# Performance work log

Hardware: AMD Instinct MI355X
Metric: run time of the kernel (lower is better)

The kernel has to match this reference:

```python
import jax, jax.numpy as jnp
import numpy as np

D = 2048; HQ = 16; HKV = 4; HD = 128
E = 8; F = 2048; FS = 11008; TOPK = 2
B = 2; S = 1024
EPS = 1e-6
NEG = -1e9


def setup_inputs() -> dict:
    key = jax.random.key(0)
    ks = jax.random.split(key, 16)
    p = lambda k, shape: jax.random.normal(k, shape, jnp.float32) * 0.02
    # rotary tables (rotate-half convention): [S, HD]
    pos = jnp.arange(S, dtype=jnp.float32)[:, None]
    inv = 1.0 / (10000.0 ** (jnp.arange(0, HD, 2, dtype=jnp.float32) / HD))
    ang = pos * inv[None, :]
    cos = jnp.concatenate([jnp.cos(ang), jnp.cos(ang)], axis=-1)
    sin = jnp.concatenate([jnp.sin(ang), jnp.sin(ang)], axis=-1)
    return dict(
        x=jax.random.normal(ks[0], (B, S, D), jnp.float32),
        rope_cos=cos, rope_sin=sin,
        attn_norm_w=jnp.ones((D,), jnp.float32),
        ffn_norm_w=jnp.ones((D,), jnp.float32),
        wq=p(ks[1], (D, HQ * HD)), bq=jnp.zeros((HQ * HD,), jnp.float32),
        wk=p(ks[2], (D, HKV * HD)), bk=jnp.zeros((HKV * HD,), jnp.float32),
        wv=p(ks[3], (D, HKV * HD)), bv=jnp.zeros((HKV * HD,), jnp.float32),
        wo=p(ks[4], (HQ * HD, D)),
        router_w=p(ks[5], (D, E)),
        w_gate=p(ks[6], (E, D, F)), w_up=p(ks[7], (E, D, F)), w_down=p(ks[8], (E, F, D)),
        ws_gate=p(ks[9], (D, FS)), ws_up=p(ks[10], (D, FS)), ws_down=p(ks[11], (FS, D)),
    )


def rmsnorm(x, w):
    return x * jax.lax.rsqrt(jnp.mean(x * x, axis=-1, keepdims=True) + EPS) * w


def rotate_half(x):
    x1, x2 = jnp.split(x, 2, axis=-1)
    return jnp.concatenate([-x2, x1], axis=-1)


def reference(x, rope_cos, rope_sin, attn_norm_w, ffn_norm_w,
              wq, bq, wk, bk, wv, bv, wo, router_w,
              w_gate, w_up, w_down, ws_gate, ws_up, ws_down):
    b, s, d = x.shape
    # ---- attention sublayer ----
    h = rmsnorm(x, attn_norm_w)
    q = (h @ wq + bq).reshape(b, s, HQ, HD)
    k = (h @ wk + bk).reshape(b, s, HKV, HD)
    v = (h @ wv + bv).reshape(b, s, HKV, HD)
    cos = rope_cos[None, :, None, :]
    sin = rope_sin[None, :, None, :]
    q = q * cos + rotate_half(q) * sin
    k = k * cos + rotate_half(k) * sin
    rep = HQ // HKV
    k = jnp.repeat(k, rep, axis=2)   # [b,s,HQ,HD]
    v = jnp.repeat(v, rep, axis=2)
    scores = jnp.einsum('bqhd,bkhd->bhqk', q, k) / np.sqrt(HD).astype(np.float32)
    causal = jnp.tril(jnp.ones((s, s), bool))
    scores = jnp.where(causal[None, None], scores, NEG)
    attn = jax.nn.softmax(scores, axis=-1)
    o = jnp.einsum('bhqk,bkhd->bqhd', attn, v).reshape(b, s, HQ * HD) @ wo
    new_k, new_v = k, v
    x = x + o
    # ---- MoE sublayer ----
    hn = rmsnorm(x, ffn_norm_w).reshape(b * s, d)   # [T,D]
    logits = hn @ router_w                           # [T,E]
    probs = jax.nn.softmax(logits, axis=-1)
    topv, topi = jax.lax.top_k(probs, TOPK)          # [T,K]
    topv = topv / jnp.sum(topv, axis=-1, keepdims=True)
    onehot = jax.nn.one_hot(topi, E, dtype=hn.dtype)  # [T,K,E]
    wdense = jnp.einsum('tke,tk->te', onehot, topv)   # sparse combine weights [T,E]
    g = jnp.einsum('td,edf->tef', hn, w_gate)
    u = jnp.einsum('td,edf->tef', hn, w_up)
    y = jnp.einsum('tef,efd->ted', jax.nn.silu(g) * u, w_down)
    routed = jnp.einsum('ted,te->td', y, wdense)
    shared = (jax.nn.silu(hn @ ws_gate) * (hn @ ws_up)) @ ws_down
    moe = (routed + shared).reshape(b, s, d)
    # load-balancing aux loss (Switch/Mixtral convention)
    frac = jnp.mean(onehot, axis=(0, 1))             # fraction dispatched per expert
    pmean = jnp.mean(probs, axis=0)
    aux_loss = E * jnp.sum(frac * pmean)
    out = x + moe
    return out, (new_k, new_v), aux_loss
```

## Files before the change

kernel.cpp:

```cpp
#include <hip/hip_runtime.h>

typedef unsigned short u16;
typedef unsigned int u32;
typedef unsigned long long u64;
typedef __attribute__((ext_vector_type(4))) unsigned short u16x4;
typedef __attribute__((ext_vector_type(8))) unsigned short u16x8;
typedef __attribute__((ext_vector_type(4))) float f32x4;
typedef __attribute__((ext_vector_type(8))) __bf16 bf16x8;

#define DD 2048
#define TT 2048
#define FSH 11008

__device__ __forceinline__ float bf2f(u16 u) {
  union { u32 i; float f; } v; v.i = ((u32)u) << 16; return v.f;
}
__device__ __forceinline__ u16 f2bf(float f) {
  union { float f; u32 i; } v; v.f = f;
  u32 r = v.i + 0x7fffu + ((v.i >> 16) & 1u);
  return (u16)(r >> 16);
}
__device__ __forceinline__ void gld16(const void* g, void* l) {
  __builtin_amdgcn_global_load_lds((const __attribute__((address_space(1))) void*)g,
                                   (__attribute__((address_space(3))) void*)l, 16, 0, 0);
}

#define MFMA16(d, a, b) d = __builtin_amdgcn_mfma_f32_16x16x32_bf16(a, b, d, 0, 0, 0)

__device__ __forceinline__ void ttile(const float* __restrict__ Wm, u16* __restrict__ Wtm,
                                      int R, int C, int n0, int k0, u16* tile, int t) {
#pragma unroll
  for (int p = 0; p < 4; ++p) {
    const int kk = (t >> 4) + p * 16;
    const int nn = (t & 15) * 4;
    float4 v = *(const float4*)(Wm + (size_t)(k0 + kk) * C + n0 + nn);
    const float vv[4] = {v.x, v.y, v.z, v.w};
#pragma unroll
    for (int j = 0; j < 4; ++j) {
      const int n = nn + j;
      tile[n * 80 + (kk ^ (((n >> 2) & 7) << 3))] = f2bf(vv[j]);
    }
  }
  __syncthreads();
#pragma unroll
  for (int p = 0; p < 2; ++p) {
    const int n = (t >> 3) + p * 32;
    const int c = t & 7;
    u16x8 v = *(const u16x8*)(tile + n * 80 + ((c * 8) ^ (((n >> 2) & 7) << 3)));
    *(u16x8*)(Wtm + (size_t)(n0 + n) * R + k0 + c * 8) = v;
  }
}

__global__ __launch_bounds__(256) void rmsnorm_k(const float* __restrict__ x,
                                                 const float* __restrict__ w,
                                                 u16* __restrict__ out) {
  const int t = threadIdx.x;
  const float* xr = x + (size_t)blockIdx.x * DD;
  float4 a = *(const float4*)(xr + t * 8);
  float4 b = *(const float4*)(xr + t * 8 + 4);
  float ss = a.x*a.x + a.y*a.y + a.z*a.z + a.w*a.w
           + b.x*b.x + b.y*b.y + b.z*b.z + b.w*b.w;
#pragma unroll
  for (int m = 1; m < 64; m <<= 1) ss += __shfl_xor(ss, m);
  __shared__ float red[4];
  if ((t & 63) == 0) red[t >> 6] = ss;
  __syncthreads();
  float sc = rsqrtf((red[0] + red[1] + red[2] + red[3]) * (1.f / DD) + 1e-6f);
  float4 wa = *(const float4*)(w + t * 8);
  float4 wb = *(const float4*)(w + t * 8 + 4);
  u16x8 o;
  o[0] = f2bf(a.x * sc * wa.x); o[1] = f2bf(a.y * sc * wa.y);
  o[2] = f2bf(a.z * sc * wa.z); o[3] = f2bf(a.w * sc * wa.w);
  o[4] = f2bf(b.x * sc * wb.x); o[5] = f2bf(b.y * sc * wb.y);
  o[6] = f2bf(b.z * sc * wb.z); o[7] = f2bf(b.w * sc * wb.w);
  *(u16x8*)(out + (size_t)blockIdx.x * DD + t * 8) = o;
}

__global__ __launch_bounds__(256) void transp_k(const float* __restrict__ W,
                                                u16* __restrict__ Wt, int R, int C) {
  __shared__ u16 tile[64 * 80];
  const size_t msz = (size_t)R * C;
  ttile(W + msz * blockIdx.z, Wt + msz * blockIdx.z, R, C,
        blockIdx.x * 64, blockIdx.y * 64, tile, threadIdx.x);
}

template <int EPI, bool SPLITK, bool EXPERT>
__global__ __launch_bounds__(512, 2) void gemm8(
    const u16* __restrict__ A, const u16* __restrict__ Bt, void* __restrict__ Cp,
    const u16* __restrict__ aux, const float* __restrict__ slotw,
    const int* __restrict__ tiletab, int M, int N, int K, int Kc) {
  __shared__ char lds[131072];
  const int t = threadIdx.x, w = t >> 6, l = t & 63;
  int m0, n0;
  if constexpr (EXPERT) {
    const int ntil = tiletab[0];
    if ((int)blockIdx.y >= ntil) return;
    const int e = tiletab[1 + blockIdx.y * 2];
    m0 = tiletab[2 + blockIdx.y * 2];
    n0 = blockIdx.x * 256;
    Bt += (size_t)e * N * K;
  } else {
    const int gx = gridDim.x, gy = gridDim.y;
    const int nwg = gx * gy;
    int wg = blockIdx.y * gx + blockIdx.x;
    wg = (wg & 7) * (nwg >> 3) + (wg >> 3);
    m0 = (wg % gy) * 256;
    n0 = (wg / gy) * 256;
  }
  int kbase = 0, KC = K;
  if constexpr (SPLITK) {
    kbase = blockIdx.z * Kc;
    const int rem = K - kbase;
    KC = rem < Kc ? rem : Kc;
  }
  const int ktiles = KC >> 6;
  const int wm = w >> 2, wn = w & 3;
  const int l15 = l & 15, l4 = l >> 4;
  const int sro = l >> 3, sc = l & 7;

  const u16* sgp[2][2][2];
  u32 sdo[2][2][2];
#pragma unroll
  for (int isB = 0; isB < 2; ++isB)
#pragma unroll
    for (int h = 0; h < 2; ++h)
#pragma unroll
      for (int i = 0; i < 2; ++i) {
        const int q = i * 8 + w;
        const int r0 = isB ? (((q >> 2) << 6) + h * 32 + (q & 3) * 8)
                           : (((q & 8) << 4) + h * 64 + (q & 7) * 8);
        const int r = r0 + sro;
        const int cl = sc ^ (r & 7);
        const u16* base = isB ? (Bt + (size_t)(n0 + r) * K) : (A + (size_t)(m0 + r) * K);
        sgp[isB][h][i] = base + kbase + cl * 8;
        sdo[isB][h][i] = (u32)(isB * 32768 + r0 * 128);
      }
  auto stage = [&](int b, int isB, int h, int kt) {
    const int kk = kt < ktiles ? kt : ktiles - 1;
#pragma unroll
    for (int i = 0; i < 2; ++i)
      gld16(sgp[isB][h][i] + kk * 64, lds + b * 65536 + sdo[isB][h][i]);
  };
  auto ldA = [&](int b, int mi, int ks) {
    const int row = wm * 128 + mi * 16 + l15;
    const int ch = (ks * 4 + l4) ^ (row & 7);
    return *(const bf16x8*)(lds + b * 65536 + row * 128 + ch * 16);
  };
  auto ldB = [&](int b, int ni, int ks) {
    const int row = wn * 64 + ni * 16 + l15;
    const int ch = (ks * 4 + l4) ^ (row & 7);
    return *(const bf16x8*)(lds + b * 65536 + 32768 + row * 128 + ch * 16);
  };

  f32x4 acc[8][4] = {};
  bf16x8 aR[4][2], b0[2][2], b1[2][2];

  stage(0, 0, 0, 0); stage(0, 1, 0, 0); stage(0, 1, 1, 0); stage(0, 0, 1, 0);
  stage(1, 0, 0, 1); stage(1, 1, 1, 1); stage(1, 0, 1, 1);
  asm volatile("s_waitcnt vmcnt(6)" ::: "memory");
  __builtin_amdgcn_s_barrier();

  for (int kt = 0; kt < ktiles; kt += 2) {
#pragma unroll
    for (int mi = 0; mi < 4; ++mi) { aR[mi][0] = ldA(0, mi, 0); aR[mi][1] = ldA(0, mi, 1); }
#pragma unroll
    for (int ni = 0; ni < 2; ++ni) { b0[ni][0] = ldB(0, ni, 0); b0[ni][1] = ldB(0, ni, 1); }
    stage(1, 1, 0, kt + 1);
    __builtin_amdgcn_s_barrier();
    asm volatile("s_waitcnt lgkmcnt(0)" ::: "memory");
    __builtin_amdgcn_s_setprio(1);
#pragma unroll
    for (int mi = 0; mi < 4; ++mi)
#pragma unroll
      for (int ni = 0; ni < 2; ++ni) {
        MFMA16(acc[mi][ni], aR[mi][0], b0[ni][0]);
        MFMA16(acc[mi][ni], aR[mi][1], b0[ni][1]);
      }
    __builtin_amdgcn_s_setprio(0);
    __builtin_amdgcn_s_barrier();
#pragma unroll
    for (int ni = 0; ni < 2; ++ni) { b1[ni][0] = ldB(0, ni + 2, 0); b1[ni][1] = ldB(0, ni + 2, 1); }
    stage(0, 0, 0, kt + 2);
    __builtin_amdgcn_s_barrier();
    asm volatile("s_waitcnt lgkmcnt(0)" ::: "memory");
    __builtin_amdgcn_s_setprio(1);
#pragma unroll
    for (int mi = 0; mi < 4; ++mi)
#pragma unroll
      for (int ni = 0; ni < 2; ++ni) {
        MFMA16(acc[mi][ni + 2], aR[mi][0], b1[ni][0]);
        MFMA16(acc[mi][ni + 2], aR[mi][1], b1[ni][1]);
      }
    __builtin_amdgcn_s_setprio(0);
    __builtin_amdgcn_s_barrier();
#pragma unroll
    for (int mi = 0; mi < 4; ++mi) { aR[mi][0] = ldA(0, mi + 4, 0); aR[mi][1] = ldA(0, mi + 4, 1); }
    stage(0, 1, 1, kt + 2);
    __builtin_amdgcn_s_barrier();
    asm volatile("s_waitcnt lgkmcnt(0)" ::: "memory");
    __builtin_amdgcn_s_setprio(1);
#pragma unroll
    for (int mi = 0; mi < 4; ++mi)
#pragma unroll
      for (int ni = 0; ni < 2; ++ni) {
        MFMA16(acc[mi + 4][ni + 2], aR[mi][0], b1[ni][0]);
        MFMA16(acc[mi + 4][ni + 2], aR[mi][1], b1[ni][1]);
      }
    __builtin_amdgcn_s_setprio(0);
    __builtin_amdgcn_s_barrier();
    stage(0, 0, 1, kt + 2);
    __builtin_amdgcn_s_barrier();
    __builtin_amdgcn_s_setprio(1);
#pragma unroll
    for (int mi = 0; mi < 4; ++mi)
#pragma unroll
      for (int ni = 0; ni < 2; ++ni) {
        MFMA16(acc[mi + 4][ni], aR[mi][0], b0[ni][0]);
        MFMA16(acc[mi + 4][ni], aR[mi][1], b0[ni][1]);
      }
    __builtin_amdgcn_s_setprio(0);
    asm volatile("s_waitcnt vmcnt(6)" ::: "memory");
    __builtin_amdgcn_s_barrier();
#pragma unroll
    for (int mi = 0; mi < 4; ++mi) { aR[mi][0] = ldA(1, mi, 0); aR[mi][1] = ldA(1, mi, 1); }
#pragma unroll
    for (int ni = 0; ni < 2; ++ni) { b0[ni][0] = ldB(1, ni, 0); b0[ni][1] = ldB(1, ni, 1); }
    stage(0, 1, 0, kt + 2);
    __builtin_amdgcn_s_barrier();
    asm volatile("s_waitcnt lgkmcnt(0)" ::: "memory");
    __builtin_amdgcn_s_setprio(1);
#pragma unroll
    for (int mi = 0; mi < 4; ++mi)
#pragma unroll
      for (int ni = 0; ni < 2; ++ni) {
        MFMA16(acc[mi][ni], aR[mi][0], b0[ni][0]);
        MFMA16(acc[mi][ni], aR[mi][1], b0[ni][1]);
      }
    __builtin_amdgcn_s_setprio(0);
    __builtin_amdgcn_s_barrier();
#pragma unroll
    for (int ni = 0; ni < 2; ++ni) { b1[ni][0] = ldB(1, ni + 2, 0); b1[ni][1] = ldB(1, ni + 2, 1); }
    stage(1, 0, 0, kt + 3);
    __builtin_amdgcn_s_barrier();
    asm volatile("s_waitcnt lgkmcnt(0)" ::: "memory");
    __builtin_amdgcn_s_setprio(1);
#pragma unroll
    for (int mi = 0; mi < 4; ++mi)
#pragma unroll
      for (int ni = 0; ni < 2; ++ni) {
        MFMA16(acc[mi][ni + 2], aR[mi][0], b1[ni][0]);
        MFMA16(acc[mi][ni + 2], aR[mi][1], b1[ni][1]);
      }
    __builtin_amdgcn_s_setprio(0);
    __builtin_amdgcn_s_barrier();
#pragma unroll
    for (int mi = 0; mi < 4; ++mi) { aR[mi][0] = ldA(1, mi + 4, 0); aR[mi][1] = ldA(1, mi + 4, 1); }
    stage(1, 1, 1, kt + 3);
    __builtin_amdgcn_s_barrier();
    asm volatile("s_waitcnt lgkmcnt(0)" ::: "memory");
    __builtin_amdgcn_s_setprio(1);
#pragma unroll
    for (int mi = 0; mi < 4; ++mi)
#pragma unroll
      for (int ni = 0; ni < 2; ++ni) {
        MFMA16(acc[mi + 4][ni + 2], aR[mi][0], b1[ni][0]);
        MFMA16(acc[mi + 4][ni + 2], aR[mi][1], b1[ni][1]);
      }
    __builtin_amdgcn_s_setprio(0);
    __builtin_amdgcn_s_barrier();
    stage(1, 0, 1, kt + 3);
    __builtin_amdgcn_s_barrier();
    __builtin_amdgcn_s_setprio(1);
#pragma unroll
    for (int mi = 0; mi < 4; ++mi)
#pragma unroll
      for (int ni = 0; ni < 2; ++ni) {
        MFMA16(acc[mi + 4][ni], aR[mi][0], b0[ni][0]);
        MFMA16(acc[mi + 4][ni], aR[mi][1], b0[ni][1]);
      }
    __builtin_amdgcn_s_setprio(0);
    asm volatile("s_waitcnt vmcnt(6)" ::: "memory");
    __builtin_amdgcn_s_barrier();
  }

  u16* C16 = (u16*)Cp;
  float* Cf = (float*)Cp;
  if constexpr (EPI == 10) C16 += (size_t)blockIdx.z * ((size_t)M * N);
  if constexpr (EPI == 11) Cf += (size_t)blockIdx.z * ((size_t)M * N);
#pragma unroll
  for (int mi = 0; mi < 8; ++mi)
#pragma unroll
    for (int rr = 0; rr < 4; ++rr) {
      const int row = m0 + wm * 128 + mi * 16 + l4 * 4 + rr;
#pragma unroll
      for (int ni = 0; ni < 4; ++ni) {
        const int col = n0 + wn * 64 + ni * 16 + l15;
        const size_t idx = (size_t)row * N + col;
        const float v = acc[mi][ni][rr];
        if constexpr (EPI == 11) {
          Cf[idx] = v;
        } else if constexpr (EPI == 3) {
          const float g = bf2f(aux[idx]);
          C16[idx] = f2bf(v * g / (1.f + __expf(-g)));
        } else if constexpr (EPI == 4) {
          C16[idx] = f2bf(slotw[row] * v);
        } else {
          C16[idx] = f2bf(v);
        }
      }
    }
}

template <bool EXPERT>
__global__ __launch_bounds__(512, 2) void gemm_gu(
    const u16* __restrict__ A, const u16* __restrict__ Btg, const u16* __restrict__ Btu,
    u16* __restrict__ act, const int* __restrict__ slot_tok, const int* __restrict__ tiletab,
    int K, int LDC) {
  __shared__ char lds[131072];
  const int t = threadIdx.x, w = t >> 6, l = t & 63;
  int m0, nt;
  const u16 *Bg, *Bu;
  if constexpr (EXPERT) {
    const int ntil = tiletab[0];
    if ((int)blockIdx.y >= ntil) return;
    const int e = tiletab[1 + blockIdx.y * 2];
    m0 = tiletab[2 + blockIdx.y * 2];
    nt = blockIdx.x;
    const size_t boff = (size_t)e * LDC * K;
    Bg = Btg + boff;
    Bu = Btu + boff;
  } else {
    const int gx = gridDim.x;
    const int nwg = gx * 8;
    int wg = blockIdx.y * gx + blockIdx.x;
    wg = (wg & 7) * (nwg >> 3) + (wg >> 3);
    m0 = (wg & 7) * 256;
    nt = wg >> 3;
    Bg = Btg;
    Bu = Btu;
  }
  const int ktiles = K >> 6;
  const int wm = w >> 2, wn = w & 3;
  const int l15 = l & 15, l4 = l >> 4;
  const int sro = l >> 3, sc = l & 7;

  const u16* sga[2][2]; u32 sda[2][2];
#pragma unroll
  for (int h = 0; h < 2; ++h)
#pragma unroll
    for (int i = 0; i < 2; ++i) {
      const int q = i * 8 + w;
      const int r0 = ((q & 8) << 4) + h * 64 + (q & 7) * 8;
      const int r = r0 + sro;
      const int cl = sc ^ (r & 7);
      size_t arow;
      if constexpr (EXPERT) arow = (size_t)slot_tok[m0 + r];
      else arow = (size_t)(m0 + r);
      sga[h][i] = A + arow * K + cl * 8;
      sda[h][i] = (u32)(r0 * 128);
    }
  const u16* sgb[2][2]; u32 sdb[2][2];
#pragma unroll
  for (int mat = 0; mat < 2; ++mat)
#pragma unroll
    for (int i = 0; i < 2; ++i) {
      const int q = i * 8 + w;
      const int r0 = q * 8;
      const int r = r0 + sro;
      const int cl = sc ^ (r & 7);
      const u16* B = mat ? Bu : Bg;
      sgb[mat][i] = B + (size_t)(nt * 128 + r) * K + cl * 8;
      sdb[mat][i] = (u32)(32768 + mat * 16384 + r0 * 128);
    }
  auto stgA = [&](int b, int h, int kt) {
    const int kk = kt < ktiles ? kt : ktiles - 1;
#pragma unroll
    for (int i = 0; i < 2; ++i) gld16(sga[h][i] + kk * 64, lds + b * 65536 + sda[h][i]);
  };
  auto stgB = [&](int b, int mat, int kt) {
    const int kk = kt < ktiles ? kt : ktiles - 1;
#pragma unroll
    for (int i = 0; i < 2; ++i) gld16(sgb[mat][i] + kk * 64, lds + b * 65536 + sdb[mat][i]);
  };
  auto ldA = [&](int b, int mi, int ks) {
    const int row = wm * 128 + mi * 16 + l15;
    const int ch = (ks * 4 + l4) ^ (row & 7);
    return *(const bf16x8*)(lds + b * 65536 + row * 128 + ch * 16);
  };
  auto ldB = [&](int b, int mat, int ni, int ks) {
    const int row = wn * 32 + ni * 16 + l15;
    const int ch = (ks * 4 + l4) ^ (row & 7);
    return *(const bf16x8*)(lds + b * 65536 + 32768 + mat * 16384 + row * 128 + ch * 16);
  };

  f32x4 accg[8][2] = {}, accu[8][2] = {};
  bf16x8 aR[4][2], bg[2][2], bu[2][2];

  stgA(0, 0, 0); stgB(0, 0, 0); stgB(0, 1, 0); stgA(0, 1, 0);
  stgA(1, 0, 1); stgB(1, 1, 1); stgA(1, 1, 1);
  asm volatile("s_waitcnt vmcnt(6)" ::: "memory");
  __builtin_amdgcn_s_barrier();

  for (int kt = 0; kt < ktiles; kt += 2) {
#pragma unroll
    for (int mi = 0; mi < 4; ++mi) { aR[mi][0] = ldA(0, mi, 0); aR[mi][1] = ldA(0, mi, 1); }
#pragma unroll
    for (int ni = 0; ni < 2; ++ni) { bg[ni][0] = ldB(0, 0, ni, 0); bg[ni][1] = ldB(0, 0, ni, 1); }
    stgB(1, 0, kt + 1);
    __builtin_amdgcn_s_barrier();
    asm volatile("s_waitcnt lgkmcnt(0)" ::: "memory");
    __builtin_amdgcn_s_setprio(1);
#pragma unroll
    for (int mi = 0; mi < 4; ++mi)
#pragma unroll
      for (int ni = 0; ni < 2; ++ni) {
        MFMA16(accg[mi][ni], aR[mi][0], bg[ni][0]);
        MFMA16(accg[mi][ni], aR[mi][1], bg[ni][1]);
      }
    __builtin_amdgcn_s_setprio(0);
    __builtin_amdgcn_s_barrier();
#pragma unroll
    for (int ni = 0; ni < 2; ++ni) { bu[ni][0] = ldB(0, 1, ni, 0); bu[ni][1] = ldB(0, 1, ni, 1); }
    stgA(0, 0, kt + 2);
    __builtin_amdgcn_s_barrier();
    asm volatile("s_waitcnt lgkmcnt(0)" ::: "memory");
    __builtin_amdgcn_s_setprio(1);
#pragma unroll
    for (int mi = 0; mi < 4; ++mi)
#pragma unroll
      for (int ni = 0; ni < 2; ++ni) {
        MFMA16(accu[mi][ni], aR[mi][0], bu[ni][0]);
        MFMA16(accu[mi][ni], aR[mi][1], bu[ni][1]);
      }
    __builtin_amdgcn_s_setprio(0);
    __builtin_amdgcn_s_barrier();
#pragma unroll
    for (int mi = 0; mi < 4; ++mi) { aR[mi][0] = ldA(0, mi + 4, 0); aR[mi][1] = ldA(0, mi + 4, 1); }
    stgB(0, 1, kt + 2);
    __builtin_amdgcn_s_barrier();
    asm volatile("s_waitcnt lgkmcnt(0)" ::: "memory");
    __builtin_amdgcn_s_setprio(1);
#pragma unroll
    for (int mi = 0; mi < 4; ++mi)
#pragma unroll
      for (int ni = 0; ni < 2; ++ni) {
        MFMA16(accu[mi + 4][ni], aR[mi][0], bu[ni][0]);
        MFMA16(accu[mi + 4][ni], aR[mi][1], bu[ni][1]);
      }
    __builtin_amdgcn_s_setprio(0);
    __builtin_amdgcn_s_barrier();
    stgA(0, 1, kt + 2);
    __builtin_amdgcn_s_barrier();
    __builtin_amdgcn_s_setprio(1);
#pragma unroll
    for (int mi = 0; mi < 4; ++mi)
#pragma unroll
      for (int ni = 0; ni < 2; ++ni) {
        MFMA16(accg[mi + 4][ni], aR[mi][0], bg[ni][0]);
        MFMA16(accg[mi + 4][ni], aR[mi][1], bg[ni][1]);
      }
    __builtin_amdgcn_s_setprio(0);
    asm volatile("s_waitcnt vmcnt(6)" ::: "memory");
    __builtin_amdgcn_s_barrier();
#pragma unroll
    for (int mi = 0; mi < 4; ++mi) { aR[mi][0] = ldA(1, mi, 0); aR[mi][1] = ldA(1, mi, 1); }
#pragma unroll
    for (int ni = 0; ni < 2; ++ni) { bg[ni][0] = ldB(1, 0, ni, 0); bg[ni][1] = ldB(1, 0, ni, 1); }
    stgB(0, 0, kt + 2);
    __builtin_amdgcn_s_barrier();
    asm volatile("s_waitcnt lgkmcnt(0)" ::: "memory");
    __builtin_amdgcn_s_setprio(1);
#pragma unroll
    for (int mi = 0; mi < 4; ++mi)
#pragma unroll
      for (int ni = 0; ni < 2; ++ni) {
        MFMA16(accg[mi][ni], aR[mi][0], bg[ni][0]);
        MFMA16(accg[mi][ni], aR[mi][1], bg[ni][1]);
      }
    __builtin_amdgcn_s_setprio(0);
    __builtin_amdgcn_s_barrier();
#pragma unroll
    for (int ni = 0; ni < 2; ++ni) { bu[ni][0] = ldB(1, 1, ni, 0); bu[ni][1] = ldB(1, 1, ni, 1); }
    stgA(1, 0, kt + 3);
    __builtin_amdgcn_s_barrier();
    asm volatile("s_waitcnt lgkmcnt(0)" ::: "memory");
    __builtin_amdgcn_s_setprio(1);
#pragma unroll
    for (int mi = 0; mi < 4; ++mi)
#pragma unroll
      for (int ni = 0; ni < 2; ++ni) {
        MFMA16(accu[mi][ni], aR[mi][0], bu[ni][0]);
        MFMA16(accu[mi][ni], aR[mi][1], bu[ni][1]);
      }
    __builtin_amdgcn_s_setprio(0);
    __builtin_amdgcn_s_barrier();
#pragma unroll
    for (int mi = 0; mi < 4; ++mi) { aR[mi][0] = ldA(1, mi + 4, 0); aR[mi][1] = ldA(1, mi + 4, 1); }
    stgB(1, 1, kt + 3);
    __builtin_amdgcn_s_barrier();
    asm volatile("s_waitcnt lgkmcnt(0)" ::: "memory");
    __builtin_amdgcn_s_setprio(1);
#pragma unroll
    for (int mi = 0; mi < 4; ++mi)
#pragma unroll
      for (int ni = 0; ni < 2; ++ni) {
        MFMA16(accu[mi + 4][ni], aR[mi][0], bu[ni][0]);
        MFMA16(accu[mi + 4][ni], aR[mi][1], bu[ni][1]);
      }
    __builtin_amdgcn_s_setprio(0);
    __builtin_amdgcn_s_barrier();
    stgA(1, 1, kt + 3);
    __builtin_amdgcn_s_barrier();
    __builtin_amdgcn_s_setprio(1);
#pragma unroll
    for (int mi = 0; mi < 4; ++mi)
#pragma unroll
      for (int ni = 0; ni < 2; ++ni) {
        MFMA16(accg[mi + 4][ni], aR[mi][0], bg[ni][0]);
        MFMA16(accg[mi + 4][ni], aR[mi][1], bg[ni][1]);
      }
    __builtin_amdgcn_s_setprio(0);
    asm volatile("s_waitcnt vmcnt(6)" ::: "memory");
    __builtin_amdgcn_s_barrier();
  }

#pragma unroll
  for (int mi = 0; mi < 8; ++mi)
#pragma unroll
    for (int rr = 0; rr < 4; ++rr) {
      const int row = m0 + wm * 128 + mi * 16 + l4 * 4 + rr;
#pragma unroll
      for (int ni = 0; ni < 2; ++ni) {
        const int col = nt * 128 + wn * 32 + ni * 16 + l15;
        const float g = accg[mi][ni][rr];
        const float u = accu[mi][ni][rr];
        act[(size_t)row * LDC + col] = f2bf(u * g / (1.f + __expf(-g)));
      }
    }
}

__global__ __launch_bounds__(256) void redbf_k(float* __restrict__ dst,
                                               const float* __restrict__ base,
                                               const u16* __restrict__ parts) {
  const int i = blockIdx.x * 256 + threadIdx.x;
  float s[8];
  const float* bp = base + (size_t)i * 8;
#pragma unroll
  for (int j = 0; j < 8; ++j) s[j] = bp[j];
#pragma unroll
  for (int p = 0; p < 4; ++p) {
    u16x8 v = ((const u16x8*)parts)[(size_t)p * 524288 + i];
#pragma unroll
    for (int j = 0; j < 8; ++j) s[j] += bf2f(v[j]);
  }
  float* dp = dst + (size_t)i * 8;
#pragma unroll
  for (int j = 0; j < 8; ++j) dp[j] = s[j];
}

__global__ __launch_bounds__(256) void rope_k(
    const u16* __restrict__ p0, const u16* __restrict__ p1,
    const float* __restrict__ cosb, const float* __restrict__ sinb,
    const float* __restrict__ bq, const float* __restrict__ bk, const float* __restrict__ bv,
    u16* __restrict__ QR, u16* __restrict__ KR, u16* __restrict__ VB,
    float* __restrict__ NK, float* __restrict__ NV) {
  const int s = blockIdx.x, b = blockIdx.y, t = threadIdx.x;
  const size_t tok = (size_t)b * 1024 + s;
  const u16* r0 = p0 + tok * 3072;
  const u16* r1 = p1 + tok * 3072;
  const float* cr = cosb + s * 128;
  const float* sr = sinb + s * 128;
  for (int i = t; i < 1024; i += 256) {
    const int h = i >> 6, d = i & 63;
    const float v1 = bf2f(r0[h * 128 + d]) + bf2f(r1[h * 128 + d]) + bq[h * 128 + d];
    const float v2 = bf2f(r0[h * 128 + d + 64]) + bf2f(r1[h * 128 + d + 64]) + bq[h * 128 + d + 64];
    const float o1 = v1 * cr[d] - v2 * sr[d];
    const float o2 = v2 * cr[d + 64] + v1 * sr[d + 64];
    const size_t qb = (((size_t)(b * 16 + h)) * 1024 + s) * 128;
    QR[qb + d] = f2bf(o1);
    QR[qb + d + 64] = f2bf(o2);
  }
  {
    const int h = t >> 6, d = t & 63;
    const float v1 = bf2f(r0[2048 + h * 128 + d]) + bf2f(r1[2048 + h * 128 + d]) + bk[h * 128 + d];
    const float v2 = bf2f(r0[2048 + h * 128 + d + 64]) + bf2f(r1[2048 + h * 128 + d + 64]) + bk[h * 128 + d + 64];
    const float o1 = v1 * cr[d] - v2 * sr[d];
    const float o2 = v2 * cr[d + 64] + v1 * sr[d + 64];
    const size_t kb = (((size_t)(b * 4 + h)) * 1024 + s) * 128;
    KR[kb + d] = f2bf(o1);
    KR[kb + d + 64] = f2bf(o2);
    const size_t ob = tok * 2048;
#pragma unroll
    for (int rep = 0; rep < 4; ++rep) {
      NK[ob + (h * 4 + rep) * 128 + d] = o1;
      NK[ob + (h * 4 + rep) * 128 + d + 64] = o2;
    }
  }
  for (int i = t; i < 512; i += 256) {
    const int h = i >> 7, d = i & 127;
    const float v = bf2f(r0[2560 + i]) + bf2f(r1[2560 + i]) + bv[i];
    VB[(((size_t)(b * 4 + h)) * 1024 + s) * 128 + d] = f2bf(v);
    const size_t ob = tok * 2048;
#pragma unroll
    for (int rep = 0; rep < 4; ++rep) NV[ob + (h * 4 + rep) * 128 + d] = v;
  }
}

__global__ __launch_bounds__(256) void attn_k(const u16* __restrict__ Q,
                                              const u16* __restrict__ Kc,
                                              const u16* __restrict__ Vc,
                                              u16* __restrict__ O,
                                              const float* __restrict__ wdsrc,
                                              u16* __restrict__ wtd) {
  __shared__ u16 Ks[64 * 128];
  __shared__ u16 Vt[128 * 66];
  __shared__ u16 Ps[4][16 * 68];
  const int t = threadIdx.x, w = t >> 6, l = t & 63;
  if (blockIdx.z == 2) {
    u16* tile = Ks;
    const int bi = blockIdx.y * 16 + blockIdx.x;
#pragma unroll 1
    for (int i = 0; i < 32; ++i) {
      const int ti = bi * 32 + i;
      const int e = ti >> 10, rem = ti & 1023;
      ttile(wdsrc + (size_t)e * 4194304, wtd + (size_t)e * 4194304,
            2048, 2048, (rem & 31) * 64, (rem >> 5) * 64, tile, t);
      __syncthreads();
    }
    return;
  }
  const int qt = blockIdx.x, h = blockIdx.y, b = blockIdx.z;
  const int kvh = h >> 2;
  const int l15 = l & 15, l4 = l >> 4;
  bf16x8 qf[4];
  {
    const u16* qb = Q + (((size_t)(b * 16 + h)) * 1024 + qt * 64 + w * 16 + l15) * 128 + l4 * 8;
#pragma unroll
    for (int c = 0; c < 4; ++c) qf[c] = *(const bf16x8*)(qb + c * 32);
  }
  float m_run[4] = {-1e30f, -1e30f, -1e30f, -1e30f};
  float l_run[4] = {0.f, 0.f, 0.f, 0.f};
  f32x4 accO[8] = {};
  const size_t kvbase = ((size_t)(b * 4 + kvh)) * 1024 * 128;
  const int ntiles = qt + 1;
  for (int kt = 0; kt < ntiles; ++kt) {
    __syncthreads();
    {
      const int key = t >> 2;
      const u16* kg = Kc + kvbase + (size_t)(kt * 64 + key) * 128;
      const u16* vg = Vc + kvbase + (size_t)(kt * 64 + key) * 128;
      const int sw = (key & 7) << 4;
#pragma unroll
      for (int p = 0; p < 4; ++p) {
        const int ch = (t & 3) * 4 + p;
        *(u16x8*)((char*)Ks + key * 256 + ((ch * 16) ^ sw)) = *(const u16x8*)(kg + ch * 8);
        const int d0 = ch * 8;
        u16x8 vv = *(const u16x8*)(vg + d0);
#pragma unroll
        for (int j = 0; j < 8; ++j) Vt[(d0 + j) * 66 + key] = vv[j];
      }
    }
    __syncthreads();
    f32x4 sf[4] = {};
    __builtin_amdgcn_s_setprio(1);
#pragma unroll
    for (int nf = 0; nf < 4; ++nf) {
      const int keyl = nf * 16 + l15;
      const int sw = (keyl & 7) << 4;
      const char* kbase = (const char*)Ks + keyl * 256;
#pragma unroll
      for (int c = 0; c < 4; ++c) {
        bf16x8 kf = *(const bf16x8*)(kbase + ((c * 64 + l4 * 16) ^ sw));
        sf[nf] = __builtin_amdgcn_mfma_f32_16x16x32_bf16(qf[c], kf, sf[nf], 0, 0, 0);
      }
    }
    __builtin_amdgcn_s_setprio(0);
    const int qg0 = qt * 64 + w * 16 + l4 * 4;
    float alpha[4];
#pragma unroll
    for (int r = 0; r < 4; ++r) {
      const int qg = qg0 + r;
      float tm = -1e30f;
#pragma unroll
      for (int nf = 0; nf < 4; ++nf) {
        const int kg = kt * 64 + nf * 16 + l15;
        float sv = sf[nf][r] * 0.088388347648318447f;
        sv = (kg <= qg) ? sv : -1e30f;
        sf[nf][r] = sv;
        tm = fmaxf(tm, sv);
      }
#pragma unroll
      for (int mm = 1; mm < 16; mm <<= 1) tm = fmaxf(tm, __shfl_xor(tm, mm));
      const float mn = fmaxf(m_run[r], tm);
      alpha[r] = __expf(m_run[r] - mn);
      m_run[r] = mn;
      float rs = 0.f;
#pragma unroll
      for (int nf = 0; nf < 4; ++nf) {
        const float p = __expf(sf[nf][r] - mn);
        sf[nf][r] = p;
        rs += p;
      }
#pragma unroll
      for (int mm = 1; mm < 16; mm <<= 1) rs += __shfl_xor(rs, mm);
      l_run[r] = l_run[r] * alpha[r] + rs;
    }
#pragma unroll
    for (int nf = 0; nf < 8; ++nf)
#pragma unroll
      for (int r = 0; r < 4; ++r) accO[nf][r] *= alpha[r];
#pragma unroll
    for (int nf = 0; nf < 4; ++nf)
#pragma unroll
      for (int r = 0; r < 4; ++r)
        Ps[w][(l4 * 4 + r) * 68 + nf * 16 + l15] = f2bf(sf[nf][r]);
    __syncthreads();
    __builtin_amdgcn_s_setprio(1);
#pragma unroll
    for (int kc = 0; kc < 2; ++kc) {
      const u16* pb = &Ps[w][0] + l15 * 68 + kc * 32 + l4 * 8;
      union { u16x4 q[2]; bf16x8 v; } pu;
      pu.q[0] = *(const u16x4*)pb;
      pu.q[1] = *(const u16x4*)(pb + 4);
#pragma unroll
      for (int nf = 0; nf < 8; ++nf) {
        const int dd = nf * 16 + l15;
        const u16* vp = &Vt[0] + dd * 66 + kc * 32 + l4 * 8;
        union { u32 u[4]; bf16x8 v; } vu;
        vu.u[0] = *(const u32*)(vp);
        vu.u[1] = *(const u32*)(vp + 2);
        vu.u[2] = *(const u32*)(vp + 4);
        vu.u[3] = *(const u32*)(vp + 6);
        accO[nf] = __builtin_amdgcn_mfma_f32_16x16x32_bf16(pu.v, vu.v, accO[nf], 0, 0, 0);
      }
    }
    __builtin_amdgcn_s_setprio(0);
  }
  const int qg0 = qt * 64 + w * 16 + l4 * 4;
#pragma unroll
  for (int nf = 0; nf < 8; ++nf) {
    const int dd = nf * 16 + l15;
#pragma unroll
    for (int r = 0; r < 4; ++r) {
      const float o = accO[nf][r] / l_run[r];
      O[((size_t)(b * 1024 + qg0 + r)) * 2048 + h * 128 + dd] = f2bf(o);
    }
  }
}

__global__ __launch_bounds__(256) void fuserouter_k(
    const float* __restrict__ x, const float* __restrict__ parts,
    const float* __restrict__ wn, const float* __restrict__ rw,
    float* __restrict__ X2, u16* __restrict__ HN,
    int* __restrict__ topi2, float* __restrict__ topw2, float* __restrict__ probs,
    const float* __restrict__ wsdsrc, u16* __restrict__ wtsd) {
  __shared__ u16 tile[64 * 80];
  __shared__ float red[4];
  __shared__ float racc[32];
  const int t = threadIdx.x, w = t >> 6;
  if ((int)blockIdx.x >= TT) {
    const int bi = blockIdx.x - TT;
#pragma unroll 1
    for (int i = 0; i < 16; ++i) {
      const int ti = bi * 16 + i;
      ttile(wsdsrc, wtsd, FSH, 2048, (ti & 31) * 64, (ti >> 5) * 64, tile, t);
      __syncthreads();
    }
    return;
  }
  const int tok = blockIdx.x;
  const size_t base = (size_t)tok * DD + t * 8;
  float v[8];
  {
    float4 a = *(const float4*)(x + base);
    float4 b = *(const float4*)(x + base + 4);
    v[0] = a.x; v[1] = a.y; v[2] = a.z; v[3] = a.w;
    v[4] = b.x; v[5] = b.y; v[6] = b.z; v[7] = b.w;
  }
#pragma unroll
  for (int p = 0; p < 4; ++p) {
    const float* pr = parts + (size_t)p * (TT * DD) + base;
    float4 a = *(const float4*)(pr);
    float4 b = *(const float4*)(pr + 4);
    v[0] += a.x; v[1] += a.y; v[2] += a.z; v[3] += a.w;
    v[4] += b.x; v[5] += b.y; v[6] += b.z; v[7] += b.w;
  }
  *(float4*)(X2 + base) = make_float4(v[0], v[1], v[2], v[3]);
  *(float4*)(X2 + base + 4) = make_float4(v[4], v[5], v[6], v[7]);
  float ss = 0.f;
#pragma unroll
  for (int j = 0; j < 8; ++j) ss += v[j] * v[j];
#pragma unroll
  for (int m = 1; m < 64; m <<= 1) ss += __shfl_xor(ss, m);
  if ((t & 63) == 0) red[w] = ss;
  __syncthreads();
  const float sc = rsqrtf((red[0] + red[1] + red[2] + red[3]) * (1.f / DD) + 1e-6f);
  float hn[8];
  u16x8 o;
#pragma unroll
  for (int j = 0; j < 8; ++j) {
    hn[j] = v[j] * sc * wn[t * 8 + j];
    o[j] = f2bf(hn[j]);
  }
  *(u16x8*)(HN + base) = o;
  float acc[8] = {};
#pragma unroll
  for (int j = 0; j < 8; ++j) {
    const int d = t * 8 + j;
    float4 r0 = *(const float4*)(rw + d * 8);
    float4 r1 = *(const float4*)(rw + d * 8 + 4);
    acc[0] += hn[j] * r0.x; acc[1] += hn[j] * r0.y; acc[2] += hn[j] * r0.z; acc[3] += hn[j] * r0.w;
    acc[4] += hn[j] * r1.x; acc[5] += hn[j] * r1.y; acc[6] += hn[j] * r1.z; acc[7] += hn[j] * r1.w;
  }
#pragma unroll
  for (int m = 1; m < 64; m <<= 1)
#pragma unroll
    for (int e = 0; e < 8; ++e) acc[e] += __shfl_xor(acc[e], m);
  if ((t & 63) == 0)
#pragma unroll
    for (int e = 0; e < 8; ++e) racc[w * 8 + e] = acc[e];
  __syncthreads();
  if (t == 0) {
    float lg[8];
#pragma unroll
    for (int e = 0; e < 8; ++e) lg[e] = racc[e] + racc[8 + e] + racc[16 + e] + racc[24 + e];
    float mx = lg[0];
#pragma unroll
    for (int e = 1; e < 8; ++e) mx = fmaxf(mx, lg[e]);
    float p[8], sum = 0.f;
#pragma unroll
    for (int e = 0; e < 8; ++e) { p[e] = __expf(lg[e] - mx); sum += p[e]; }
    const float inv = 1.f / sum;
#pragma unroll
    for (int e = 0; e < 8; ++e) p[e] *= inv;
    *(float4*)(probs + tok * 8) = make_float4(p[0], p[1], p[2], p[3]);
    *(float4*)(probs + tok * 8 + 4) = make_float4(p[4], p[5], p[6], p[7]);
    int e0 = 0; float v0 = p[0];
#pragma unroll
    for (int e = 1; e < 8; ++e) if (p[e] > v0) { v0 = p[e]; e0 = e; }
    int e1 = (e0 == 0) ? 1 : 0; float v1 = p[e1];
#pragma unroll
    for (int e = 0; e < 8; ++e) if (e != e0 && p[e] > v1) { v1 = p[e]; e1 = e; }
    const float wsum = v0 + v1;
    topi2[tok * 2] = e0; topi2[tok * 2 + 1] = e1;
    topw2[tok * 2] = v0 / wsum; topw2[tok * 2 + 1] = v1 / wsum;
  }
}

__global__ __launch_bounds__(256) void zero_k(int* __restrict__ slot_tok,
                                              float* __restrict__ slot_w) {
  const int i = blockIdx.x * 256 + threadIdx.x;
  if (i < 6144) { slot_tok[i] = 0; slot_w[i] = 0.f; }
}

__global__ __launch_bounds__(256) void scan2_k(const int* __restrict__ topi2,
                                               const float* __restrict__ probs,
                                               int* __restrict__ cursors,
                                               int* __restrict__ tiletab,
                                               float* __restrict__ auxout) {
  const int t = threadIdx.x, w = t >> 6, l = t & 63;
  __shared__ int cnt[8];
  __shared__ float wsum[4][8];
  if (t < 8) cnt[t] = 0;
  __syncthreads();
  float ps[8] = {};
  for (int i = t; i < 2048; i += 256) {
    atomicAdd(&cnt[topi2[i * 2]], 1);
    atomicAdd(&cnt[topi2[i * 2 + 1]], 1);
    float4 a = *(const float4*)(probs + i * 8);
    float4 b = *(const float4*)(probs + i * 8 + 4);
    ps[0] += a.x; ps[1] += a.y; ps[2] += a.z; ps[3] += a.w;
    ps[4] += b.x; ps[5] += b.y; ps[6] += b.z; ps[7] += b.w;
  }
#pragma unroll
  for (int m = 1; m < 64; m <<= 1)
#pragma unroll
    for (int e = 0; e < 8; ++e) ps[e] += __shfl_xor(ps[e], m);
  if (l == 0)
#pragma unroll
    for (int e = 0; e < 8; ++e) wsum[w][e] = ps[e];
  __syncthreads();
  if (t == 0) {
    int off = 0, nt = 0;
    float aux = 0.f;
    for (int e = 0; e < 8; ++e) {
      cursors[e] = off;
      const int c = cnt[e];
      const int nte = (c + 255) >> 8;
      for (int i = 0; i < nte; ++i) {
        tiletab[1 + nt * 2] = e;
        tiletab[2 + nt * 2] = off + i * 256;
        ++nt;
      }
      off += nte * 256;
      const float pm = (wsum[0][e] + wsum[1][e] + wsum[2][e] + wsum[3][e]) * (1.f / 2048.f);
      aux += ((float)c * (1.f / 4096.f)) * pm;
    }
    tiletab[0] = nt;
    *auxout = 8.f * aux;
  }
}

__global__ __launch_bounds__(256) void assign_k(const int* __restrict__ topi2,
                                                const float* __restrict__ topw2,
                                                int* __restrict__ cursors,
                                                int* __restrict__ slot_tok,
                                                float* __restrict__ slot_w,
                                                int* __restrict__ tok_slot) {
  __shared__ int lcnt[8];
  __shared__ int base[8];
  const int t = threadIdx.x;
  const int tok = blockIdx.x * 256 + t;
  if (t < 8) lcnt[t] = 0;
  __syncthreads();
  int e[2], lr[2];
#pragma unroll
  for (int j = 0; j < 2; ++j) {
    e[j] = topi2[tok * 2 + j];
    lr[j] = atomicAdd(&lcnt[e[j]], 1);
  }
  __syncthreads();
  if (t < 8) base[t] = atomicAdd(&cursors[t], lcnt[t]);
  __syncthreads();
#pragma unroll
  for (int j = 0; j < 2; ++j) {
    const int s = base[e[j]] + lr[j];
    slot_tok[s] = tok;
    slot_w[s] = topw2[tok * 2 + j];
    tok_slot[tok * 2 + j] = s;
  }
}

__global__ __launch_bounds__(256) void final_k(float* __restrict__ out,
                                               const u16* __restrict__ routed,
                                               const int* __restrict__ tok_slot) {
  const int tok = blockIdx.x, t = threadIdx.x;
  const int s0 = tok_slot[tok * 2], s1 = tok_slot[tok * 2 + 1];
  u16x8 a = ((const u16x8*)(routed + (size_t)s0 * DD))[t];
  u16x8 b = ((const u16x8*)(routed + (size_t)s1 * DD))[t];
  float* o = out + (size_t)tok * DD + t * 8;
  float4 o0 = *(const float4*)o;
  float4 o1 = *(const float4*)(o + 4);
  o0.x += bf2f(a[0]) + bf2f(b[0]); o0.y += bf2f(a[1]) + bf2f(b[1]);
  o0.z += bf2f(a[2]) + bf2f(b[2]); o0.w += bf2f(a[3]) + bf2f(b[3]);
  o1.x += bf2f(a[4]) + bf2f(b[4]); o1.y += bf2f(a[5]) + bf2f(b[5]);
  o1.z += bf2f(a[6]) + bf2f(b[6]); o1.w += bf2f(a[7]) + bf2f(b[7]);
  *(float4*)o = o0;
  *(float4*)(o + 4) = o1;
}

extern "C" void kernel_launch(void* const* d_in, const int* in_sizes, int n_in,
                              void* d_out, int out_size, void* d_ws, size_t ws_size,
                              hipStream_t stream) {
  (void)in_sizes; (void)n_in; (void)out_size; (void)ws_size;
  const float* x    = (const float*)d_in[0];
  const float* rc   = (const float*)d_in[1];
  const float* rs   = (const float*)d_in[2];
  const float* anw  = (const float*)d_in[3];
  const float* fnw  = (const float*)d_in[4];
  const float* wq   = (const float*)d_in[5];
  const float* bq   = (const float*)d_in[6];
  const float* wk   = (const float*)d_in[7];
  const float* bk   = (const float*)d_in[8];
  const float* wv   = (const float*)d_in[9];
  const float* bv   = (const float*)d_in[10];
  const float* wo   = (const float*)d_in[11];
  const float* rw   = (const float*)d_in[12];
  const float* wg   = (const float*)d_in[13];
  const float* wu   = (const float*)d_in[14];
  const float* wd   = (const float*)d_in[15];
  const float* wsg  = (const float*)d_in[16];
  const float* wsu  = (const float*)d_in[17];
  const float* wsd  = (const float*)d_in[18];

  const size_t MB = (size_t)1 << 20;
  char* ws = (char*)d_ws;
  float* X2     = (float*)(ws + 0);
  u16*   HN     = (u16*)(ws + 16 * MB);
  char*  SM     = ws + 24 * MB;
  u16*   H      = (u16*)(ws + 25 * MB);
  u16*   WTQ    = (u16*)(ws + 33 * MB);
  u16*   PARTSQ = (u16*)(ws + 46 * MB);
  u16*   QR     = (u16*)(ws + 72 * MB);
  u16*   KR     = (u16*)(ws + 80 * MB);
  u16*   VBb    = (u16*)(ws + 82 * MB);
  u16*   ATTNO  = (u16*)(ws + 84 * MB);
  u16*   WTO    = (u16*)(ws + 92 * MB);
  float* PARTSW = (float*)(ws + 100 * MB);
  u16*   WTSg   = (u16*)(ws + 164 * MB);
  u16*   WTSu   = (u16*)(ws + 208 * MB);
  u16*   G      = (u16*)(ws + 252 * MB);
  u16*   WTSd   = (u16*)(ws + 296 * MB);
  u16*   PARTSD = (u16*)(ws + 340 * MB);
  u16*   WTEg   = (u16*)(ws + 372 * MB);
  u16*   WTEu   = (u16*)(ws + 436 * MB);
  u16*   WTEd   = (u16*)(ws + 500 * MB);
  u16*   ACT    = (u16*)(ws + 564 * MB);
  u16*   ROUTED = (u16*)(ws + 588 * MB);

  int*   CURS  = (int*)(SM + 256);
  int*   TILT  = (int*)(SM + 512);
  int*   TOPI  = (int*)(SM + 4096);
  float* TOPW  = (float*)(SM + 40960);
  int*   STOK  = (int*)(SM + 73728);
  float* SW    = (float*)(SM + 98304);
  int*   TSLOT = (int*)(SM + 131072);
  float* PROBS = (float*)(SM + 163840);

  float* out  = (float*)d_out;
  float* NK   = out + 4194304;
  float* NV   = out + 2 * 4194304;
  float* AUXO = out + 3 * 4194304;

  const dim3 b256(256);
  const dim3 b512(512);

  rmsnorm_k<<<TT, b256, 0, stream>>>(x, anw, H);
  transp_k<<<dim3(32, 32, 1), b256, 0, stream>>>(wq, WTQ, 2048, 2048);
  transp_k<<<dim3(8, 32, 1), b256, 0, stream>>>(wk, WTQ + (size_t)2048 * 2048, 2048, 512);
  transp_k<<<dim3(8, 32, 1), b256, 0, stream>>>(wv, WTQ + (size_t)2560 * 2048, 2048, 512);
  gemm8<10, true, false><<<dim3(12, 8, 2), b512, 0, stream>>>(
      H, WTQ, PARTSQ, nullptr, nullptr, nullptr, TT, 3072, 2048, 1024);
  rope_k<<<dim3(1024, 2), b256, 0, stream>>>(PARTSQ, PARTSQ + (size_t)TT * 3072, rc, rs,
                                             bq, bk, bv, QR, KR, VBb, NK, NV);
  attn_k<<<dim3(16, 16, 3), b256, 0, stream>>>(QR, KR, VBb, ATTNO, wd, WTEd);
  transp_k<<<dim3(32, 32, 1), b256, 0, stream>>>(wo, WTO, 2048, 2048);
  gemm8<11, true, false><<<dim3(8, 8, 4), b512, 0, stream>>>(
      ATTNO, WTO, PARTSW, nullptr, nullptr, nullptr, TT, 2048, 2048, 512);
  zero_k<<<24, b256, 0, stream>>>(STOK, SW);
  fuserouter_k<<<TT + 344, b256, 0, stream>>>(x, PARTSW, fnw, rw, X2, HN, TOPI, TOPW, PROBS,
                                              wsd, WTSd);
  scan2_k<<<1, b256, 0, stream>>>(TOPI, PROBS, CURS, TILT, AUXO);
  assign_k<<<8, b256, 0, stream>>>(TOPI, TOPW, CURS, STOK, SW, TSLOT);
  transp_k<<<dim3(172, 32, 1), b256, 0, stream>>>(wsg, WTSg, 2048, FSH);
  transp_k<<<dim3(172, 32, 1), b256, 0, stream>>>(wsu, WTSu, 2048, FSH);
  gemm_gu<false><<<dim3(86, 8, 1), b512, 0, stream>>>(
      HN, WTSg, WTSu, G, nullptr, nullptr, 2048, FSH);
  gemm8<10, true, false><<<dim3(8, 8, 4), b512, 0, stream>>>(
      G, WTSd, PARTSD, nullptr, nullptr, nullptr, TT, 2048, FSH, 2816);
  redbf_k<<<2048, b256, 0, stream>>>(out, X2, PARTSD);
  transp_k<<<dim3(32, 32, 8), b256, 0, stream>>>(wg, WTEg, 2048, 2048);
  transp_k<<<dim3(32, 32, 8), b256, 0, stream>>>(wu, WTEu, 2048, 2048);
  gemm_gu<true><<<dim3(16, 24, 1), b512, 0, stream>>>(
      HN, WTEg, WTEu, ACT, STOK, TILT, 2048, 2048);
  gemm8<4, false, true><<<dim3(8, 24, 1), b512, 0, stream>>>(
      ACT, WTEd, ROUTED, nullptr, SW, TILT, 0, 2048, 2048, 0);
  final_k<<<TT, b256, 0, stream>>>(out, ROUTED, TSLOT);
}
```

Before: 836.1 us.

## Fold weight transposes into rmsnorm, rope and attention kernels as side blocks

```diff
diff --git a/kernel.cpp b/kernel.cpp
--- a/kernel.cpp
+++ b/kernel.cpp
@@ -53,8 +53,32 @@
 
 __global__ __launch_bounds__(256) void rmsnorm_k(const float* __restrict__ x,
                                                  const float* __restrict__ w,
-                                                 u16* __restrict__ out) {
+                                                 u16* __restrict__ out,
+                                                 const float* __restrict__ wq,
+                                                 const float* __restrict__ wk,
+                                                 const float* __restrict__ wv,
+                                                 u16* __restrict__ WTQ) {
+  __shared__ u16 tile[64 * 80];
+  __shared__ float red[4];
   const int t = threadIdx.x;
+  if ((int)blockIdx.x >= TT) {
+    const int bi = blockIdx.x - TT;
+#pragma unroll 1
+    for (int i = 0; i < 8; ++i) {
+      const int ti = bi * 8 + i;
+      if (ti < 1024) {
+        ttile(wq, WTQ, 2048, 2048, (ti & 31) * 64, (ti >> 5) * 64, tile, t);
+      } else if (ti < 1280) {
+        const int r = ti - 1024;
+        ttile(wk, WTQ + (size_t)2048 * 2048, 2048, 512, (r & 7) * 64, (r >> 3) * 64, tile, t);
+      } else {
+        const int r = ti - 1280;
+        ttile(wv, WTQ + (size_t)2560 * 2048, 2048, 512, (r & 7) * 64, (r >> 3) * 64, tile, t);
+      }
+      __syncthreads();
+    }
+    return;
+  }
   const float* xr = x + (size_t)blockIdx.x * DD;
   float4 a = *(const float4*)(xr + t * 8);
   float4 b = *(const float4*)(xr + t * 8 + 4);
@@ -62,7 +86,6 @@
            + b.x*b.x + b.y*b.y + b.z*b.z + b.w*b.w;
 #pragma unroll
   for (int m = 1; m < 64; m <<= 1) ss += __shfl_xor(ss, m);
-  __shared__ float red[4];
   if ((t & 63) == 0) red[t >> 6] = ss;
   __syncthreads();
   float sc = rsqrtf((red[0] + red[1] + red[2] + red[3]) * (1.f / DD) + 1e-6f);
@@ -74,14 +97,6 @@
   o[4] = f2bf(b.x * sc * wb.x); o[5] = f2bf(b.y * sc * wb.y);
   o[6] = f2bf(b.z * sc * wb.z); o[7] = f2bf(b.w * sc * wb.w);
   *(u16x8*)(out + (size_t)blockIdx.x * DD + t * 8) = o;
-}
-
-__global__ __launch_bounds__(256) void transp_k(const float* __restrict__ W,
-                                                u16* __restrict__ Wt, int R, int C) {
-  __shared__ u16 tile[64 * 80];
-  const size_t msz = (size_t)R * C;
-  ttile(W + msz * blockIdx.z, Wt + msz * blockIdx.z, R, C,
-        blockIdx.x * 64, blockIdx.y * 64, tile, threadIdx.x);
 }
 
 template <int EPI, bool SPLITK, bool EXPERT>
@@ -563,8 +578,28 @@
     const float* __restrict__ cosb, const float* __restrict__ sinb,
     const float* __restrict__ bq, const float* __restrict__ bk, const float* __restrict__ bv,
     u16* __restrict__ QR, u16* __restrict__ KR, u16* __restrict__ VB,
-    float* __restrict__ NK, float* __restrict__ NV) {
-  const int s = blockIdx.x, b = blockIdx.y, t = threadIdx.x;
+    float* __restrict__ NK, float* __restrict__ NV,
+    const float* __restrict__ wsg, const float* __restrict__ wsu,
+    u16* __restrict__ WTSg, u16* __restrict__ WTSu) {
+  __shared__ u16 tile[64 * 80];
+  const int t = threadIdx.x;
+  if (blockIdx.y == 2) {
+    const int bi = blockIdx.x;
+#pragma unroll 1
+    for (int i = 0; i < 11; ++i) {
+      const int ti = bi * 11 + i;
+      if (ti >= 11008) break;
+      if (ti < 5504) {
+        ttile(wsg, WTSg, 2048, FSH, (ti % 172) * 64, (ti / 172) * 64, tile, t);
+      } else {
+        const int r = ti - 5504;
+        ttile(wsu, WTSu, 2048, FSH, (r % 172) * 64, (r / 172) * 64, tile, t);
+      }
+      __syncthreads();
+    }
+    return;
+  }
+  const int s = blockIdx.x, b = blockIdx.y;
   const size_t tok = (size_t)b * 1024 + s;
   const u16* r0 = p0 + tok * 3072;
   const u16* r1 = p1 + tok * 3072;
@@ -610,22 +645,35 @@
                                               const u16* __restrict__ Kc,
                                               const u16* __restrict__ Vc,
                                               u16* __restrict__ O,
-                                              const float* __restrict__ wdsrc,
-                                              u16* __restrict__ wtd) {
+                                              const float* __restrict__ wdsrc, u16* __restrict__ wtd,
+                                              const float* __restrict__ wgsrc, u16* __restrict__ wtg,
+                                              const float* __restrict__ wusrc, u16* __restrict__ wtu,
+                                              const float* __restrict__ wosrc, u16* __restrict__ wto) {
   __shared__ u16 Ks[64 * 128];
   __shared__ u16 Vt[128 * 66];
   __shared__ u16 Ps[4][16 * 68];
   const int t = threadIdx.x, w = t >> 6, l = t & 63;
-  if (blockIdx.z == 2) {
+  if (blockIdx.z >= 2) {
     u16* tile = Ks;
     const int bi = blockIdx.y * 16 + blockIdx.x;
+    if (blockIdx.z <= 4) {
+      const float* src = blockIdx.z == 2 ? wdsrc : (blockIdx.z == 3 ? wgsrc : wusrc);
+      u16* dst = blockIdx.z == 2 ? wtd : (blockIdx.z == 3 ? wtg : wtu);
 #pragma unroll 1
-    for (int i = 0; i < 32; ++i) {
-      const int ti = bi * 32 + i;
-      const int e = ti >> 10, rem = ti & 1023;
-      ttile(wdsrc + (size_t)e * 4194304, wtd + (size_t)e * 4194304,
-            2048, 2048, (rem & 31) * 64, (rem >> 5) * 64, tile, t);
-      __syncthreads();
+      for (int i = 0; i < 32; ++i) {
+        const int ti = bi * 32 + i;
+        const int e = ti >> 10, rem = ti & 1023;
+        ttile(src + (size_t)e * 4194304, dst + (size_t)e * 4194304,
+              2048, 2048, (rem & 31) * 64, (rem >> 5) * 64, tile, t);
+        __syncthreads();
+      }
+    } else {
+#pragma unroll 1
+      for (int i = 0; i < 4; ++i) {
+        const int ti = bi * 4 + i;
+        ttile(wosrc, wto, 2048, 2048, (ti & 31) * 64, (ti >> 5) * 64, tile, t);
+        __syncthreads();
+      }
     }
     return;
   }
@@ -1015,16 +1063,14 @@
   const dim3 b256(256);
   const dim3 b512(512);
 
-  rmsnorm_k<<<TT, b256, 0, stream>>>(x, anw, H);
-  transp_k<<<dim3(32, 32, 1), b256, 0, stream>>>(wq, WTQ, 2048, 2048);
-  transp_k<<<dim3(8, 32, 1), b256, 0, stream>>>(wk, WTQ + (size_t)2048 * 2048, 2048, 512);
-  transp_k<<<dim3(8, 32, 1), b256, 0, stream>>>(wv, WTQ + (size_t)2560 * 2048, 2048, 512);
+  rmsnorm_k<<<TT + 192, b256, 0, stream>>>(x, anw, H, wq, wk, wv, WTQ);
   gemm8<10, true, false><<<dim3(12, 8, 2), b512, 0, stream>>>(
       H, WTQ, PARTSQ, nullptr, nullptr, nullptr, TT, 3072, 2048, 1024);
-  rope_k<<<dim3(1024, 2), b256, 0, stream>>>(PARTSQ, PARTSQ + (size_t)TT * 3072, rc, rs,
-                                             bq, bk, bv, QR, KR, VBb, NK, NV);
-  attn_k<<<dim3(16, 16, 3), b256, 0, stream>>>(QR, KR, VBb, ATTNO, wd, WTEd);
-  transp_k<<<dim3(32, 32, 1), b256, 0, stream>>>(wo, WTO, 2048, 2048);
+  rope_k<<<dim3(1024, 3), b256, 0, stream>>>(PARTSQ, PARTSQ + (size_t)TT * 3072, rc, rs,
+                                             bq, bk, bv, QR, KR, VBb, NK, NV,
+                                             wsg, wsu, WTSg, WTSu);
+  attn_k<<<dim3(16, 16, 6), b256, 0, stream>>>(QR, KR, VBb, ATTNO,
+                                               wd, WTEd, wg, WTEg, wu, WTEu, wo, WTO);
   gemm8<11, true, false><<<dim3(8, 8, 4), b512, 0, stream>>>(
       ATTNO, WTO, PARTSW, nullptr, nullptr, nullptr, TT, 2048, 2048, 512);
   zero_k<<<24, b256, 0, stream>>>(STOK, SW);
@@ -1032,15 +1078,11 @@
                                               wsd, WTSd);
   scan2_k<<<1, b256, 0, stream>>>(TOPI, PROBS, CURS, TILT, AUXO);
   assign_k<<<8, b256, 0, stream>>>(TOPI, TOPW, CURS, STOK, SW, TSLOT);
-  transp_k<<<dim3(172, 32, 1), b256, 0, stream>>>(wsg, WTSg, 2048, FSH);
-  transp_k<<<dim3(172, 32, 1), b256, 0, stream>>>(wsu, WTSu, 2048, FSH);
   gemm_gu<false><<<dim3(86, 8, 1), b512, 0, stream>>>(
       HN, WTSg, WTSu, G, nullptr, nullptr, 2048, FSH);
   gemm8<10, true, false><<<dim3(8, 8, 4), b512, 0, stream>>>(
       G, WTSd, PARTSD, nullptr, nullptr, nullptr, TT, 2048, FSH, 2816);
   redbf_k<<<2048, b256, 0, stream>>>(out, X2, PARTSD);
-  transp_k<<<dim3(32, 32, 8), b256, 0, stream>>>(wg, WTEg, 2048, 2048);
-  transp_k<<<dim3(32, 32, 8), b256, 0, stream>>>(wu, WTEu, 2048, 2048);
   gemm_gu<true><<<dim3(16, 24, 1), b512, 0, stream>>>(
       HN, WTEg, WTEu, ACT, STOK, TILT, 2048, 2048);
   gemm8<4, false, true><<<dim3(8, 24, 1), b512, 0, stream>>>(
```

Measured after the change: 870.2 us. +4.1%, slower.

## Merge shared and routed-expert gate/up GEMMs into a single launch

Applied to the files above, without the earlier changes.

```diff
diff --git a/kernel.cpp b/kernel.cpp
--- a/kernel.cpp
+++ b/kernel.cpp
@@ -311,33 +311,35 @@
     }
 }
 
-template <bool EXPERT>
-__global__ __launch_bounds__(512, 2) void gemm_gu(
-    const u16* __restrict__ A, const u16* __restrict__ Btg, const u16* __restrict__ Btu,
-    u16* __restrict__ act, const int* __restrict__ slot_tok, const int* __restrict__ tiletab,
-    int K, int LDC) {
+__global__ __launch_bounds__(512, 2) void gemm_gu_m(
+    const u16* __restrict__ A,
+    const u16* __restrict__ Bsg, const u16* __restrict__ Bsu, u16* __restrict__ G,
+    const u16* __restrict__ Beg, const u16* __restrict__ Beu, u16* __restrict__ ACT,
+    const int* __restrict__ slot_tok, const int* __restrict__ tiletab, int K) {
   __shared__ char lds[131072];
   const int t = threadIdx.x, w = t >> 6, l = t & 63;
-  int m0, nt;
+  int m0, nt, LDC;
   const u16 *Bg, *Bu;
-  if constexpr (EXPERT) {
-    const int ntil = tiletab[0];
-    if ((int)blockIdx.y >= ntil) return;
-    const int e = tiletab[1 + blockIdx.y * 2];
-    m0 = tiletab[2 + blockIdx.y * 2];
-    nt = blockIdx.x;
-    const size_t boff = (size_t)e * LDC * K;
-    Bg = Btg + boff;
-    Bu = Btu + boff;
-  } else {
-    const int gx = gridDim.x;
-    const int nwg = gx * 8;
-    int wg = blockIdx.y * gx + blockIdx.x;
-    wg = (wg & 7) * (nwg >> 3) + (wg >> 3);
+  u16* dst;
+  bool expertp;
+  if ((int)blockIdx.y < 8) {
+    expertp = false;
+    int wg = blockIdx.y * 86 + blockIdx.x;
+    wg = (wg & 7) * 86 + (wg >> 3);
     m0 = (wg & 7) * 256;
     nt = wg >> 3;
-    Bg = Btg;
-    Bu = Btu;
+    Bg = Bsg; Bu = Bsu; dst = G; LDC = FSH;
+  } else {
+    expertp = true;
+    if ((int)blockIdx.x >= 16) return;
+    const int ntil = tiletab[0];
+    const int ty = blockIdx.y - 8;
+    if (ty >= ntil) return;
+    const int e = tiletab[1 + ty * 2];
+    m0 = tiletab[2 + ty * 2];
+    nt = blockIdx.x;
+    const size_t boff = (size_t)e * 2048 * K;
+    Bg = Beg + boff; Bu = Beu + boff; dst = ACT; LDC = 2048;
   }
   const int ktiles = K >> 6;
   const int wm = w >> 2, wn = w & 3;
@@ -353,9 +355,7 @@
       const int r0 = ((q & 8) << 4) + h * 64 + (q & 7) * 8;
       const int r = r0 + sro;
       const int cl = sc ^ (r & 7);
-      size_t arow;
-      if constexpr (EXPERT) arow = (size_t)slot_tok[m0 + r];
-      else arow = (size_t)(m0 + r);
+      const size_t arow = expertp ? (size_t)slot_tok[m0 + r] : (size_t)(m0 + r);
       sga[h][i] = A + arow * K + cl * 8;
       sda[h][i] = (u32)(r0 * 128);
     }
@@ -534,7 +534,7 @@
         const int col = nt * 128 + wn * 32 + ni * 16 + l15;
         const float g = accg[mi][ni][rr];
         const float u = accu[mi][ni][rr];
-        act[(size_t)row * LDC + col] = f2bf(u * g / (1.f + __expf(-g)));
+        dst[(size_t)row * LDC + col] = f2bf(u * g / (1.f + __expf(-g)));
       }
     }
 }
@@ -1034,15 +1034,13 @@
   assign_k<<<8, b256, 0, stream>>>(TOPI, TOPW, CURS, STOK, SW, TSLOT);
   transp_k<<<dim3(172, 32, 1), b256, 0, stream>>>(wsg, WTSg, 2048, FSH);
   transp_k<<<dim3(172, 32, 1), b256, 0, stream>>>(wsu, WTSu, 2048, FSH);
-  gemm_gu<false><<<dim3(86, 8, 1), b512, 0, stream>>>(
-      HN, WTSg, WTSu, G, nullptr, nullptr, 2048, FSH);
+  transp_k<<<dim3(32, 32, 8), b256, 0, stream>>>(wg, WTEg, 2048, 2048);
+  transp_k<<<dim3(32, 32, 8), b256, 0, stream>>>(wu, WTEu, 2048, 2048);
+  gemm_gu_m<<<dim3(86, 32, 1), b512, 0, stream>>>(
+      HN, WTSg, WTSu, G, WTEg, WTEu, ACT, STOK, TILT, 2048);
   gemm8<10, true, false><<<dim3(8, 8, 4), b512, 0, stream>>>(
       G, WTSd, PARTSD, nullptr, nullptr, nullptr, TT, 2048, FSH, 2816);
   redbf_k<<<2048, b256, 0, stream>>>(out, X2, PARTSD);
-  transp_k<<<dim3(32, 32, 8), b256, 0, stream>>>(wg, WTEg, 2048, 2048);
-  transp_k<<<dim3(32, 32, 8), b256, 0, stream>>>(wu, WTEu, 2048, 2048);
-  gemm_gu<true><<<dim3(16, 24, 1), b512, 0, stream>>>(
-      HN, WTEg, WTEu, ACT, STOK, TILT, 2048, 2048);
   gemm8<4, false, true><<<dim3(8, 24, 1), b512, 0, stream>>>(
       ACT, WTEd, ROUTED, nullptr, SW, TILT, 0, 2048, 2048, 0);
   final_k<<<TT, b256, 0, stream>>>(out, ROUTED, TSLOT);
```

Measured after the change: 845.9 us. Within noise of the previous version (+1.2%).
